# Optimization experiments

Measured on AMD Instinct MI355X. Metric: run time of the kernel, lower is better.

## Reference

```python
import jax, jax.numpy as jnp
import numpy as np

B, H, S, D = 2, 16, 2048, 64

def setup_inputs() -> dict:
    key = jax.random.key(0)
    kq, kk, kv = jax.random.split(key, 3)
    query = jax.random.normal(kq, (B, H, S, D), dtype=jnp.float32)
    key_t = jax.random.normal(kk, (B, H, S, D), dtype=jnp.float32)
    value = jax.random.normal(kv, (B, H, S, D), dtype=jnp.float32)
    return {"query": query, "key": key_t, "value": value}

def reference(query, key, value):
    d_k = query.shape[-1]
    scale = 1.0 / jnp.sqrt(jnp.asarray(d_k, dtype=query.dtype))
    # scores: [B, H, S, S]
    scores = jnp.einsum('bhqd,bhkd->bhqk', query, key) * scale
    p_attn = jax.nn.softmax(scores, axis=-1)
    output = jnp.einsum('bhqk,bhkd->bhqd', p_attn, value)
    return (output, p_attn)
```

## Files before the change

### kernel.cpp

```cpp
#include <hip/hip_runtime.h>

#define SS 2048
#define DD 64
#define QB 128
#define KVB 64
#define NT (SS / KVB)

typedef unsigned short ushort_t;
typedef __attribute__((ext_vector_type(4)))  float f32x4;
typedef __attribute__((ext_vector_type(16))) float f32x16;
typedef __attribute__((ext_vector_type(8)))  short bf16x8;
typedef __attribute__((ext_vector_type(2)))  unsigned int u32x2;

static __device__ __forceinline__ unsigned short f2bf(float f) {
    unsigned u = __builtin_bit_cast(unsigned, f);
    u += 0x7FFFu + ((u >> 16) & 1u);
    return (unsigned short)(u >> 16);
}

static __device__ __forceinline__ f32x16 zero16() {
    f32x16 z;
#pragma unroll
    for (int i = 0; i < 16; ++i) z[i] = 0.f;
    return z;
}

union PFrag { bf16x8 v; unsigned w[4]; };

#define GLL16(src, dst) \
    __builtin_amdgcn_global_load_lds((const __attribute__((address_space(1))) void*)(src), \
                                     (__attribute__((address_space(3))) void*)(dst), 16, 0, 0)

__global__ void cvt_bf16(const float* __restrict__ src, ushort_t* __restrict__ dst,
                         int n8, float scale)
{
    int i = blockIdx.x * blockDim.x + threadIdx.x;
    if (i >= n8) return;
    f32x4 a = ((const f32x4*)src)[2 * i];
    f32x4 b = ((const f32x4*)src)[2 * i + 1];
    bf16x8 o;
#pragma unroll
    for (int j = 0; j < 4; ++j) o[j] = (short)f2bf(a[j] * scale);
#pragma unroll
    for (int j = 0; j < 4; ++j) o[4 + j] = (short)f2bf(b[j] * scale);
    ((bf16x8*)dst)[i] = o;
}

__global__ void transposeV(const float* __restrict__ V, ushort_t* __restrict__ Vt)
{
    __shared__ float tile[64][65];
    const int tid = threadIdx.x;
    const int hh = blockIdx.x >> 5;
    const int kt = blockIdx.x & 31;

#pragma unroll
    for (int it = 0; it < 4; ++it) {
        int m = it * 256 + tid;
        int r = m >> 4, c4 = m & 15;
        f32x4 v = *(const f32x4*)(V + ((size_t)(hh * SS + kt * 64 + r)) * DD + c4 * 4);
#pragma unroll
        for (int j = 0; j < 4; ++j) tile[r][c4 * 4 + j] = v[j];
    }
    __syncthreads();
#pragma unroll
    for (int it = 0; it < 2; ++it) {
        int m = it * 256 + tid;
        int d = m >> 3, c8 = m & 7;
        bf16x8 o;
#pragma unroll
        for (int j = 0; j < 8; ++j) o[j] = (short)f2bf(tile[c8 * 8 + j][d]);
        *(bf16x8*)(Vt + ((size_t)hh * DD + d) * SS + kt * 64 + c8 * 8) = o;
    }
}

__global__ __launch_bounds__(256, 2)
void attn_main(const ushort_t* __restrict__ Qbf, const ushort_t* __restrict__ Kbf,
               const ushort_t* __restrict__ Vtbf, float* __restrict__ gO,
               float* __restrict__ gP)
{
    __shared__ ushort_t lds[2][8192];

    const int tid  = threadIdx.x;
    const int lane = tid & 63;
    const int wave = tid >> 6;
    const int lo5  = lane & 31;
    const int hi   = lane >> 5;

    const int bid  = blockIdx.x;
    const int wg   = (bid & 7) * 64 + (bid >> 3);
    const int head = wg >> 4;
    const int q0b  = (wg & 15) * QB;

    const ushort_t* Qh = Qbf  + (size_t)head * SS * DD;
    const ushort_t* Kh = Kbf  + (size_t)head * SS * DD;
    const ushort_t* Vh = Vtbf + (size_t)head * DD * SS;
    float* Oh = gO + (size_t)head * SS * DD;
    float* Ph = gP + (size_t)head * SS * SS;

    const int qg = q0b + wave * 32 + lo5;
    bf16x8 qf[4];
#pragma unroll
    for (int ks = 0; ks < 4; ++ks)
        qf[ks] = *(const bf16x8*)(Qh + (size_t)qg * DD + ks * 16 + hi * 8);

    const int lgrp = lane >> 3;
    const int lchk = (lane & 7) ^ lgrp;
    const ushort_t* srcK[2], *srcV[2];
    ushort_t* dK[2][2], *dV[2][2];
#pragma unroll
    for (int j = 0; j < 2; ++j) {
        int W = wave * 2 + j;
        srcK[j] = Kh + (size_t)(W * 8 + lgrp) * DD + lchk * 8;
        srcV[j] = Vh + (size_t)(W * 8 + lgrp) * SS + lchk * 8;
#pragma unroll
        for (int b = 0; b < 2; ++b) {
            dK[b][j] = &lds[b][W * 512];
            dV[b][j] = &lds[b][4096 + W * 512];
        }
    }

#pragma unroll
    for (int j = 0; j < 2; ++j) GLL16(srcK[j], dK[0][j]);
    __syncthreads();

    float lsum0 = 0.f, lsum1 = 0.f;
    int buf = 0;
    for (int t = 0; t < NT; ++t) {
        if (t + 1 < NT) {
#pragma unroll
            for (int j = 0; j < 2; ++j)
                GLL16(srcK[j] + (size_t)(t + 1) * KVB * DD, dK[buf ^ 1][j]);
        }
        const ushort_t* Ksb = &lds[buf][0];
#pragma unroll
        for (int sub = 0; sub < 2; ++sub) {
            f32x16 acc = zero16();
            int kvl = sub * 32 + lo5;
#pragma unroll
            for (int ks = 0; ks < 4; ++ks) {
                bf16x8 kf = *(const bf16x8*)(Ksb + kvl * 64 + ((((ks * 2) + hi) ^ (kvl & 7)) << 3));
                acc = __builtin_amdgcn_mfma_f32_32x32x16_bf16(kf, qf[ks], acc, 0, 0, 0);
            }
#pragma unroll
            for (int r = 0; r < 16; r += 2) {
                lsum0 += __builtin_exp2f(acc[r]);
                lsum1 += __builtin_exp2f(acc[r + 1]);
            }
        }
        __syncthreads();
        buf ^= 1;
    }
    float l_run = lsum0 + lsum1;
    l_run += __shfl_xor(l_run, 32);
    const float rinv = 1.0f / l_run;

    f32x16 o0 = zero16(), o1 = zero16();
    float* prow_base = Ph + (size_t)qg * SS;

#pragma unroll
    for (int j = 0; j < 2; ++j) { GLL16(srcK[j], dK[0][j]); GLL16(srcV[j], dV[0][j]); }
    __syncthreads();

    buf = 0;
    for (int t = 0; t < NT; ++t) {
        if (t + 1 < NT) {
#pragma unroll
            for (int j = 0; j < 2; ++j) {
                GLL16(srcK[j] + (size_t)(t + 1) * KVB * DD, dK[buf ^ 1][j]);
                GLL16(srcV[j] + (size_t)(t + 1) * KVB,      dV[buf ^ 1][j]);
            }
        }
        const ushort_t* Ksb = &lds[buf][0];
        const ushort_t* Vtb = &lds[buf][4096];
#pragma unroll
        for (int sub = 0; sub < 2; ++sub) {
            f32x16 acc = zero16();
            int kvl = sub * 32 + lo5;
#pragma unroll
            for (int ks = 0; ks < 4; ++ks) {
                bf16x8 kf = *(const bf16x8*)(Ksb + kvl * 64 + ((((ks * 2) + hi) ^ (kvl & 7)) << 3));
                acc = __builtin_amdgcn_mfma_f32_32x32x16_bf16(kf, qf[ks], acc, 0, 0, 0);
            }
            float pr[16];
#pragma unroll
            for (int r = 0; r < 16; ++r) pr[r] = __builtin_exp2f(acc[r]);

            float* prow = prow_base + t * KVB + sub * 32;
#pragma unroll
            for (int g = 0; g < 4; ++g) {
                f32x4 st = { pr[4*g+0] * rinv, pr[4*g+1] * rinv, pr[4*g+2] * rinv, pr[4*g+3] * rinv };
                *(f32x4*)(prow + g * 8 + hi * 4) = st;
            }

            unsigned u[8];
#pragma unroll
            for (int j = 0; j < 8; ++j)
                u[j] = (unsigned)f2bf(pr[2*j]) | ((unsigned)f2bf(pr[2*j+1]) << 16);

            unsigned s0 = __shfl_xor(u[0], 32), s1 = __shfl_xor(u[1], 32);
            unsigned s2 = __shfl_xor(u[2], 32), s3 = __shfl_xor(u[3], 32);
            unsigned s4 = __shfl_xor(u[4], 32), s5 = __shfl_xor(u[5], 32);
            unsigned s6 = __shfl_xor(u[6], 32), s7 = __shfl_xor(u[7], 32);
            PFrag pf0, pf1;
            pf0.w[0] = hi ? s2 : u[0];  pf0.w[1] = hi ? s3 : u[1];
            pf0.w[2] = hi ? u[2] : s0;  pf0.w[3] = hi ? u[3] : s1;
            pf1.w[0] = hi ? s6 : u[4];  pf1.w[1] = hi ? s7 : u[5];
            pf1.w[2] = hi ? u[6] : s4;  pf1.w[3] = hi ? u[7] : s5;

#pragma unroll
            for (int dt = 0; dt < 2; ++dt) {
                int drow = dt * 32 + lo5;
                int c0 = ((sub * 4) + 0 + hi) ^ (drow & 7);
                int c1 = ((sub * 4) + 2 + hi) ^ (drow & 7);
                bf16x8 vf0 = *(const bf16x8*)(Vtb + drow * 64 + (c0 << 3));
                bf16x8 vf1 = *(const bf16x8*)(Vtb + drow * 64 + (c1 << 3));
                f32x16& od = dt ? o1 : o0;
                od = __builtin_amdgcn_mfma_f32_32x32x16_bf16(vf0, pf0.v, od, 0, 0, 0);
                od = __builtin_amdgcn_mfma_f32_32x32x16_bf16(vf1, pf1.v, od, 0, 0, 0);
            }
        }
        __syncthreads();
        buf ^= 1;
    }

    float* orow = Oh + (size_t)qg * DD;
#pragma unroll
    for (int dt = 0; dt < 2; ++dt) {
        const f32x16& od = dt ? o1 : o0;
#pragma unroll
        for (int g = 0; g < 4; ++g) {
            f32x4 st = { od[4*g+0] * rinv, od[4*g+1] * rinv, od[4*g+2] * rinv, od[4*g+3] * rinv };
            *(f32x4*)(orow + dt * 32 + g * 8 + hi * 4) = st;
        }
    }
}

__global__ __launch_bounds__(256, 2)
void attn_fused(const float* __restrict__ gQ, const float* __restrict__ gK,
                const float* __restrict__ gV, float* __restrict__ gO,
                float* __restrict__ gP)
{
    __shared__ unsigned short Qs[QB * DD];
    __shared__ unsigned short Ks[KVB * DD];
    __shared__ unsigned short Vt[DD * KVB];

    const int tid  = threadIdx.x;
    const int lane = tid & 63;
    const int wave = tid >> 6;
    const int lo5  = lane & 31;
    const int hi   = lane >> 5;

    const int head = blockIdx.x >> 4;
    const int qblk = blockIdx.x & 15;
    const int q0b  = qblk * QB;

    const float* Qh = gQ + (size_t)head * SS * DD;
    const float* Kh = gK + (size_t)head * SS * DD;
    const float* Vh = gV + (size_t)head * SS * DD;
    float* Oh = gO + (size_t)head * SS * DD;
    float* Ph = gP + (size_t)head * SS * SS;

    const float SCALE = 0.125f * 1.44269504088896340736f;

#pragma unroll
    for (int it = 0; it < 8; ++it) {
        int m = it * 256 + tid;
        int q = m >> 4, d4 = m & 15;
        f32x4 v = *(const f32x4*)(Qh + (size_t)(q0b + q) * DD + d4 * 4);
        unsigned a = (unsigned)f2bf(v.x * SCALE) | ((unsigned)f2bf(v.y * SCALE) << 16);
        unsigned b = (unsigned)f2bf(v.z * SCALE) | ((unsigned)f2bf(v.w * SCALE) << 16);
        u32x2 w; w.x = a; w.y = b;
        *(u32x2*)(Qs + q * 64 + d4 * 4) = w;
    }
    __syncthreads();

    const int qrow = wave * 32 + lo5;
    bf16x8 qf[4];
#pragma unroll
    for (int ks = 0; ks < 4; ++ks)
        qf[ks] = *(const bf16x8*)(Qs + qrow * 64 + ks * 16 + hi * 8);

    auto stageK = [&](int kv0) {
#pragma unroll
        for (int it = 0; it < 4; ++it) {
            int m = it * 256 + tid;
            int kv = m >> 4, d4 = m & 15;
            f32x4 v = *(const f32x4*)(Kh + (size_t)(kv0 + kv) * DD + d4 * 4);
            unsigned a = (unsigned)f2bf(v.x) | ((unsigned)f2bf(v.y) << 16);
            unsigned b = (unsigned)f2bf(v.z) | ((unsigned)f2bf(v.w) << 16);
            int c16 = (d4 >> 1) ^ (kv & 7);
            u32x2 w; w.x = a; w.y = b;
            *(u32x2*)(Ks + kv * 64 + c16 * 8 + (d4 & 1) * 4) = w;
        }
    };
    auto stageV = [&](int kv0) {
#pragma unroll
        for (int it = 0; it < 2; ++it) {
            int m = it * 256 + tid;
            int kv2 = m >> 4, d4 = m & 15;
            const float* p0 = Vh + (size_t)(kv0 + kv2 * 2) * DD + d4 * 4;
            f32x4 v0 = *(const f32x4*)(p0);
            f32x4 v1 = *(const f32x4*)(p0 + DD);
#pragma unroll
            for (int c = 0; c < 4; ++c) {
                int d = d4 * 4 + c;
                unsigned u = (unsigned)f2bf(v0[c]) | ((unsigned)f2bf(v1[c]) << 16);
                int c16 = (kv2 >> 2) ^ (d & 7);
                *(unsigned*)(Vt + d * 64 + c16 * 8 + (kv2 & 3) * 2) = u;
            }
        }
    };

    float m_run = -1e30f, l_run = 0.f;
    for (int kv0 = 0; kv0 < SS; kv0 += KVB) {
        __syncthreads();
        stageK(kv0);
        __syncthreads();
#pragma unroll
        for (int sub = 0; sub < 2; ++sub) {
            f32x16 acc = zero16();
            int kvl = sub * 32 + lo5;
#pragma unroll
            for (int ks = 0; ks < 4; ++ks) {
                bf16x8 kf = *(const bf16x8*)(Ks + kvl * 64 + ((((ks * 2) + hi) ^ (kvl & 7)) << 3));
                acc = __builtin_amdgcn_mfma_f32_32x32x16_bf16(kf, qf[ks], acc, 0, 0, 0);
            }
            float tm = acc[0];
#pragma unroll
            for (int r = 1; r < 16; ++r) tm = fmaxf(tm, acc[r]);
            float mn = fmaxf(m_run, tm);
            float sum = 0.f;
#pragma unroll
            for (int r = 0; r < 16; ++r) sum += __builtin_exp2f(acc[r] - mn);
            l_run = l_run * __builtin_exp2f(m_run - mn) + sum;
            m_run = mn;
        }
    }
    {
        float mo = __shfl_xor(m_run, 32);
        float mf = fmaxf(m_run, mo);
        float la = l_run * __builtin_exp2f(m_run - mf);
        float lb = __shfl_xor(la, 32);
        l_run = la + lb;
        m_run = mf;
    }
    const float rinv = 1.0f / l_run;

    f32x16 o0 = zero16(), o1 = zero16();
    const int qg = q0b + wave * 32 + lo5;
    float* prow_base = Ph + (size_t)qg * SS;

    for (int kv0 = 0; kv0 < SS; kv0 += KVB) {
        __syncthreads();
        stageK(kv0);
        stageV(kv0);
        __syncthreads();
#pragma unroll
        for (int sub = 0; sub < 2; ++sub) {
            f32x16 acc = zero16();
            int kvl = sub * 32 + lo5;
#pragma unroll
            for (int ks = 0; ks < 4; ++ks) {
                bf16x8 kf = *(const bf16x8*)(Ks + kvl * 64 + ((((ks * 2) + hi) ^ (kvl & 7)) << 3));
                acc = __builtin_amdgcn_mfma_f32_32x32x16_bf16(kf, qf[ks], acc, 0, 0, 0);
            }
            float pr[16];
#pragma unroll
            for (int r = 0; r < 16; ++r) pr[r] = __builtin_exp2f(acc[r] - m_run);

            float* prow = prow_base + kv0 + sub * 32;
#pragma unroll
            for (int g = 0; g < 4; ++g) {
                f32x4 st = { pr[4*g+0] * rinv, pr[4*g+1] * rinv, pr[4*g+2] * rinv, pr[4*g+3] * rinv };
                *(f32x4*)(prow + g * 8 + hi * 4) = st;
            }

            unsigned u[8];
#pragma unroll
            for (int j = 0; j < 8; ++j)
                u[j] = (unsigned)f2bf(pr[2*j]) | ((unsigned)f2bf(pr[2*j+1]) << 16);

            unsigned s0 = __shfl_xor(u[0], 32), s1 = __shfl_xor(u[1], 32);
            unsigned s2 = __shfl_xor(u[2], 32), s3 = __shfl_xor(u[3], 32);
            unsigned s4 = __shfl_xor(u[4], 32), s5 = __shfl_xor(u[5], 32);
            unsigned s6 = __shfl_xor(u[6], 32), s7 = __shfl_xor(u[7], 32);
            PFrag pf0, pf1;
            pf0.w[0] = hi ? s2 : u[0];  pf0.w[1] = hi ? s3 : u[1];
            pf0.w[2] = hi ? u[2] : s0;  pf0.w[3] = hi ? u[3] : s1;
            pf1.w[0] = hi ? s6 : u[4];  pf1.w[1] = hi ? s7 : u[5];
            pf1.w[2] = hi ? u[6] : s4;  pf1.w[3] = hi ? u[7] : s5;

#pragma unroll
            for (int dt = 0; dt < 2; ++dt) {
                int drow = dt * 32 + lo5;
                int c0 = ((sub * 4) + 0 + hi) ^ (drow & 7);
                int c1 = ((sub * 4) + 2 + hi) ^ (drow & 7);
                bf16x8 vf0 = *(const bf16x8*)(Vt + drow * 64 + (c0 << 3));
                bf16x8 vf1 = *(const bf16x8*)(Vt + drow * 64 + (c1 << 3));
                f32x16& od = dt ? o1 : o0;
                od = __builtin_amdgcn_mfma_f32_32x32x16_bf16(vf0, pf0.v, od, 0, 0, 0);
                od = __builtin_amdgcn_mfma_f32_32x32x16_bf16(vf1, pf1.v, od, 0, 0, 0);
            }
        }
    }

    float* orow = Oh + (size_t)qg * DD;
#pragma unroll
    for (int dt = 0; dt < 2; ++dt) {
        const f32x16& od = dt ? o1 : o0;
#pragma unroll
        for (int g = 0; g < 4; ++g) {
            f32x4 st = { od[4*g+0] * rinv, od[4*g+1] * rinv, od[4*g+2] * rinv, od[4*g+3] * rinv };
            *(f32x4*)(orow + dt * 32 + g * 8 + hi * 4) = st;
        }
    }
}

extern "C" void kernel_launch(void* const* d_in, const int* in_sizes, int n_in,
                              void* d_out, int out_size, void* d_ws, size_t ws_size,
                              hipStream_t stream) {
    const float* Q = (const float*)d_in[0];
    const float* K = (const float*)d_in[1];
    const float* V = (const float*)d_in[2];
    float* O = (float*)d_out;
    float* P = O + (size_t)2 * 16 * SS * DD;

    const size_t HD = (size_t)32 * SS * DD;
    const size_t need = 3 * HD * sizeof(ushort_t);
    const float SCALE = 0.125f * 1.44269504088896340736f;

    if (ws_size >= need) {
        ushort_t* wsp  = (ushort_t*)d_ws;
        ushort_t* Qbf  = wsp;
        ushort_t* Kbf  = wsp + HD;
        ushort_t* Vtbf = wsp + 2 * HD;
        int n8 = (int)(HD / 8);
        hipLaunchKernelGGL(cvt_bf16, dim3(n8 / 256), dim3(256), 0, stream, Q, Qbf, n8, SCALE);
        hipLaunchKernelGGL(cvt_bf16, dim3(n8 / 256), dim3(256), 0, stream, K, Kbf, n8, 1.0f);
        hipLaunchKernelGGL(transposeV, dim3(1024), dim3(256), 0, stream, V, Vtbf);
        hipLaunchKernelGGL(attn_main, dim3(512), dim3(256), 0, stream, Qbf, Kbf, Vtbf, O, P);
    } else {
        hipLaunchKernelGGL(attn_fused, dim3(512), dim3(256), 0, stream, Q, K, V, O, P);
    }
}
```

Measured before the change: 215.2 us.

## Split KV range across waves with LDS reduction and fuse Q conversion

The main attention kernel now gives each block 32 query rows, and its four waves each take a quarter of the KV sequence. Softmax denominators and partial outputs are combined through LDS at the end. K and V fragments are read directly from global memory instead of through a double-buffered global_load_lds pipeline. Q bf16 conversion and scaling move inside the kernel, which drops a separate conversion launch, and P stores become nontemporal. The launch uses 2048 blocks with a 3-blocks-per-CU bound to raise parallelism, at the cost of uncached-by-LDS direct global K/V reads and an extra cross-wave reduction.

```diff
diff --git a/kernel.cpp b/kernel.cpp
--- a/kernel.cpp
+++ b/kernel.cpp
@@ -2,9 +2,6 @@
 
 #define SS 2048
 #define DD 64
-#define QB 128
-#define KVB 64
-#define NT (SS / KVB)
 
 typedef unsigned short ushort_t;
 typedef __attribute__((ext_vector_type(4)))  float f32x4;
@@ -26,10 +23,6 @@
 }
 
 union PFrag { bf16x8 v; unsigned w[4]; };
-
-#define GLL16(src, dst) \
-    __builtin_amdgcn_global_load_lds((const __attribute__((address_space(1))) void*)(src), \
-                                     (__attribute__((address_space(3))) void*)(dst), 16, 0, 0)
 
 __global__ void cvt_bf16(const float* __restrict__ src, ushort_t* __restrict__ dst,
                          int n8, float scale)
@@ -73,12 +66,13 @@
     }
 }
 
-__global__ __launch_bounds__(256, 2)
-void attn_main(const ushort_t* __restrict__ Qbf, const ushort_t* __restrict__ Kbf,
-               const ushort_t* __restrict__ Vtbf, float* __restrict__ gO,
-               float* __restrict__ gP)
+__global__ __launch_bounds__(256, 3)
+void attn_main2(const float* __restrict__ gQ, const ushort_t* __restrict__ Kbf,
+                const ushort_t* __restrict__ Vtbf, float* __restrict__ gO,
+                float* __restrict__ gP)
 {
-    __shared__ ushort_t lds[2][8192];
+    __shared__ float lsm[4 * 32];
+    __shared__ float osm[4 * 64 * 33];
 
     const int tid  = threadIdx.x;
     const int lane = tid & 63;
@@ -87,109 +81,85 @@
     const int hi   = lane >> 5;
 
     const int bid  = blockIdx.x;
-    const int wg   = (bid & 7) * 64 + (bid >> 3);
-    const int head = wg >> 4;
-    const int q0b  = (wg & 15) * QB;
-
-    const ushort_t* Qh = Qbf  + (size_t)head * SS * DD;
+    const int wg   = (bid & 7) * 256 + (bid >> 3);
+    const int head = wg >> 6;
+    const int q0b  = (wg & 63) * 32;
+
+    const float*    Qh = gQ   + (size_t)head * SS * DD;
     const ushort_t* Kh = Kbf  + (size_t)head * SS * DD;
     const ushort_t* Vh = Vtbf + (size_t)head * DD * SS;
     float* Oh = gO + (size_t)head * SS * DD;
     float* Ph = gP + (size_t)head * SS * SS;
 
-    const int qg = q0b + wave * 32 + lo5;
+    const float SCALE = 0.125f * 1.44269504088896340736f;
+
+    const int qrow = q0b + lo5;
     bf16x8 qf[4];
 #pragma unroll
-    for (int ks = 0; ks < 4; ++ks)
-        qf[ks] = *(const bf16x8*)(Qh + (size_t)qg * DD + ks * 16 + hi * 8);
-
-    const int lgrp = lane >> 3;
-    const int lchk = (lane & 7) ^ lgrp;
-    const ushort_t* srcK[2], *srcV[2];
-    ushort_t* dK[2][2], *dV[2][2];
-#pragma unroll
-    for (int j = 0; j < 2; ++j) {
-        int W = wave * 2 + j;
-        srcK[j] = Kh + (size_t)(W * 8 + lgrp) * DD + lchk * 8;
-        srcV[j] = Vh + (size_t)(W * 8 + lgrp) * SS + lchk * 8;
-#pragma unroll
-        for (int b = 0; b < 2; ++b) {
-            dK[b][j] = &lds[b][W * 512];
-            dV[b][j] = &lds[b][4096 + W * 512];
-        }
-    }
-
-#pragma unroll
-    for (int j = 0; j < 2; ++j) GLL16(srcK[j], dK[0][j]);
-    __syncthreads();
-
-    float lsum0 = 0.f, lsum1 = 0.f;
-    int buf = 0;
-    for (int t = 0; t < NT; ++t) {
-        if (t + 1 < NT) {
-#pragma unroll
-            for (int j = 0; j < 2; ++j)
-                GLL16(srcK[j] + (size_t)(t + 1) * KVB * DD, dK[buf ^ 1][j]);
-        }
-        const ushort_t* Ksb = &lds[buf][0];
+    for (int ks = 0; ks < 4; ++ks) {
+        const float* qp = Qh + (size_t)qrow * DD + ks * 16 + hi * 8;
+        f32x4 a = *(const f32x4*)(qp);
+        f32x4 b = *(const f32x4*)(qp + 4);
+        bf16x8 o;
+#pragma unroll
+        for (int j = 0; j < 4; ++j) o[j] = (short)f2bf(a[j] * SCALE);
+#pragma unroll
+        for (int j = 0; j < 4; ++j) o[4 + j] = (short)f2bf(b[j] * SCALE);
+        qf[ks] = o;
+    }
+
+    const int kv_base = wave * 512;
+
+    float ls0 = 0.f, ls1 = 0.f;
+#pragma unroll 2
+    for (int t = 0; t < 8; ++t) {
+        int kv0 = kv_base + t * 64;
 #pragma unroll
         for (int sub = 0; sub < 2; ++sub) {
             f32x16 acc = zero16();
-            int kvl = sub * 32 + lo5;
+            const ushort_t* kp = Kh + (size_t)(kv0 + sub * 32 + lo5) * DD + hi * 8;
 #pragma unroll
             for (int ks = 0; ks < 4; ++ks) {
-                bf16x8 kf = *(const bf16x8*)(Ksb + kvl * 64 + ((((ks * 2) + hi) ^ (kvl & 7)) << 3));
+                bf16x8 kf = *(const bf16x8*)(kp + ks * 16);
                 acc = __builtin_amdgcn_mfma_f32_32x32x16_bf16(kf, qf[ks], acc, 0, 0, 0);
             }
 #pragma unroll
             for (int r = 0; r < 16; r += 2) {
-                lsum0 += __builtin_exp2f(acc[r]);
-                lsum1 += __builtin_exp2f(acc[r + 1]);
-            }
-        }
-        __syncthreads();
-        buf ^= 1;
-    }
-    float l_run = lsum0 + lsum1;
-    l_run += __shfl_xor(l_run, 32);
-    const float rinv = 1.0f / l_run;
+                ls0 += __builtin_exp2f(acc[r]);
+                ls1 += __builtin_exp2f(acc[r + 1]);
+            }
+        }
+    }
+    float lsum = ls0 + ls1;
+    lsum += __shfl_xor(lsum, 32);
+    lsm[wave * 32 + lo5] = lsum;
+    __syncthreads();
+    const float rinv = 1.0f / (lsm[lo5] + lsm[32 + lo5] + lsm[64 + lo5] + lsm[96 + lo5]);
 
     f32x16 o0 = zero16(), o1 = zero16();
-    float* prow_base = Ph + (size_t)qg * SS;
-
-#pragma unroll
-    for (int j = 0; j < 2; ++j) { GLL16(srcK[j], dK[0][j]); GLL16(srcV[j], dV[0][j]); }
-    __syncthreads();
-
-    buf = 0;
-    for (int t = 0; t < NT; ++t) {
-        if (t + 1 < NT) {
-#pragma unroll
-            for (int j = 0; j < 2; ++j) {
-                GLL16(srcK[j] + (size_t)(t + 1) * KVB * DD, dK[buf ^ 1][j]);
-                GLL16(srcV[j] + (size_t)(t + 1) * KVB,      dV[buf ^ 1][j]);
-            }
-        }
-        const ushort_t* Ksb = &lds[buf][0];
-        const ushort_t* Vtb = &lds[buf][4096];
+    float* prow_base = Ph + (size_t)qrow * SS;
+
+#pragma unroll 2
+    for (int t = 0; t < 8; ++t) {
+        int kv0 = kv_base + t * 64;
 #pragma unroll
         for (int sub = 0; sub < 2; ++sub) {
             f32x16 acc = zero16();
-            int kvl = sub * 32 + lo5;
+            const ushort_t* kp = Kh + (size_t)(kv0 + sub * 32 + lo5) * DD + hi * 8;
 #pragma unroll
             for (int ks = 0; ks < 4; ++ks) {
-                bf16x8 kf = *(const bf16x8*)(Ksb + kvl * 64 + ((((ks * 2) + hi) ^ (kvl & 7)) << 3));
+                bf16x8 kf = *(const bf16x8*)(kp + ks * 16);
                 acc = __builtin_amdgcn_mfma_f32_32x32x16_bf16(kf, qf[ks], acc, 0, 0, 0);
             }
             float pr[16];
 #pragma unroll
             for (int r = 0; r < 16; ++r) pr[r] = __builtin_exp2f(acc[r]);
 
-            float* prow = prow_base + t * KVB + sub * 32;
+            float* prow = prow_base + kv0 + sub * 32;
 #pragma unroll
             for (int g = 0; g < 4; ++g) {
                 f32x4 st = { pr[4*g+0] * rinv, pr[4*g+1] * rinv, pr[4*g+2] * rinv, pr[4*g+3] * rinv };
-                *(f32x4*)(prow + g * 8 + hi * 4) = st;
+                __builtin_nontemporal_store(st, (f32x4*)(prow + g * 8 + hi * 4));
             }
 
             unsigned u[8];
@@ -209,29 +179,46 @@
 
 #pragma unroll
             for (int dt = 0; dt < 2; ++dt) {
-                int drow = dt * 32 + lo5;
-                int c0 = ((sub * 4) + 0 + hi) ^ (drow & 7);
-                int c1 = ((sub * 4) + 2 + hi) ^ (drow & 7);
-                bf16x8 vf0 = *(const bf16x8*)(Vtb + drow * 64 + (c0 << 3));
-                bf16x8 vf1 = *(const bf16x8*)(Vtb + drow * 64 + (c1 << 3));
+                const ushort_t* vp = Vh + (size_t)(dt * 32 + lo5) * SS + kv0 + sub * 32 + hi * 8;
+                bf16x8 vf0 = *(const bf16x8*)(vp);
+                bf16x8 vf1 = *(const bf16x8*)(vp + 16);
                 f32x16& od = dt ? o1 : o0;
                 od = __builtin_amdgcn_mfma_f32_32x32x16_bf16(vf0, pf0.v, od, 0, 0, 0);
                 od = __builtin_amdgcn_mfma_f32_32x32x16_bf16(vf1, pf1.v, od, 0, 0, 0);
             }
         }
-        __syncthreads();
-        buf ^= 1;
-    }
-
-    float* orow = Oh + (size_t)qg * DD;
+    }
+
 #pragma unroll
     for (int dt = 0; dt < 2; ++dt) {
         const f32x16& od = dt ? o1 : o0;
 #pragma unroll
         for (int g = 0; g < 4; ++g) {
-            f32x4 st = { od[4*g+0] * rinv, od[4*g+1] * rinv, od[4*g+2] * rinv, od[4*g+3] * rinv };
-            *(f32x4*)(orow + dt * 32 + g * 8 + hi * 4) = st;
-        }
+#pragma unroll
+            for (int j = 0; j < 4; ++j) {
+                int d = dt * 32 + g * 8 + hi * 4 + j;
+                osm[(wave * 64 + d) * 33 + lo5] = od[4 * g + j];
+            }
+        }
+    }
+    __syncthreads();
+
+    {
+        const int q  = tid >> 3;
+        const int d0 = (tid & 7) * 8;
+        const float rq = 1.0f / (lsm[q] + lsm[32 + q] + lsm[64 + q] + lsm[96 + q]);
+        float out[8];
+#pragma unroll
+        for (int i = 0; i < 8; ++i) {
+            int d = d0 + i;
+            out[i] = (osm[(0 * 64 + d) * 33 + q] + osm[(1 * 64 + d) * 33 + q] +
+                      osm[(2 * 64 + d) * 33 + q] + osm[(3 * 64 + d) * 33 + q]) * rq;
+        }
+        float* op = Oh + (size_t)(q0b + q) * DD + d0;
+        f32x4 a = { out[0], out[1], out[2], out[3] };
+        f32x4 b = { out[4], out[5], out[6], out[7] };
+        *(f32x4*)(op)     = a;
+        *(f32x4*)(op + 4) = b;
     }
 }
 
@@ -240,9 +227,9 @@
                 const float* __restrict__ gV, float* __restrict__ gO,
                 float* __restrict__ gP)
 {
-    __shared__ unsigned short Qs[QB * DD];
-    __shared__ unsigned short Ks[KVB * DD];
-    __shared__ unsigned short Vt[DD * KVB];
+    __shared__ unsigned short Qs[128 * DD];
+    __shared__ unsigned short Ks[64 * DD];
+    __shared__ unsigned short Vt[DD * 64];
 
     const int tid  = threadIdx.x;
     const int lane = tid & 63;
@@ -251,8 +238,7 @@
     const int hi   = lane >> 5;
 
     const int head = blockIdx.x >> 4;
-    const int qblk = blockIdx.x & 15;
-    const int q0b  = qblk * QB;
+    const int q0b  = (blockIdx.x & 15) * 128;
 
     const float* Qh = gQ + (size_t)head * SS * DD;
     const float* Kh = gK + (size_t)head * SS * DD;
@@ -312,7 +298,7 @@
     };
 
     float m_run = -1e30f, l_run = 0.f;
-    for (int kv0 = 0; kv0 < SS; kv0 += KVB) {
+    for (int kv0 = 0; kv0 < SS; kv0 += 64) {
         __syncthreads();
         stageK(kv0);
         __syncthreads();
@@ -350,7 +336,7 @@
     const int qg = q0b + wave * 32 + lo5;
     float* prow_base = Ph + (size_t)qg * SS;
 
-    for (int kv0 = 0; kv0 < SS; kv0 += KVB) {
+    for (int kv0 = 0; kv0 < SS; kv0 += 64) {
         __syncthreads();
         stageK(kv0);
         stageV(kv0);
@@ -426,19 +412,15 @@
     float* P = O + (size_t)2 * 16 * SS * DD;
 
     const size_t HD = (size_t)32 * SS * DD;
-    const size_t need = 3 * HD * sizeof(ushort_t);
-    const float SCALE = 0.125f * 1.44269504088896340736f;
+    const size_t need = 2 * HD * sizeof(ushort_t);
 
     if (ws_size >= need) {
-        ushort_t* wsp  = (ushort_t*)d_ws;
-        ushort_t* Qbf  = wsp;
-        ushort_t* Kbf  = wsp + HD;
-        ushort_t* Vtbf = wsp + 2 * HD;
+        ushort_t* Kbf  = (ushort_t*)d_ws;
+        ushort_t* Vtbf = Kbf + HD;
         int n8 = (int)(HD / 8);
-        hipLaunchKernelGGL(cvt_bf16, dim3(n8 / 256), dim3(256), 0, stream, Q, Qbf, n8, SCALE);
         hipLaunchKernelGGL(cvt_bf16, dim3(n8 / 256), dim3(256), 0, stream, K, Kbf, n8, 1.0f);
         hipLaunchKernelGGL(transposeV, dim3(1024), dim3(256), 0, stream, V, Vtbf);
-        hipLaunchKernelGGL(attn_main, dim3(512), dim3(256), 0, stream, Qbf, Kbf, Vtbf, O, P);
+        hipLaunchKernelGGL(attn_main2, dim3(2048), dim3(256), 0, stream, Q, Kbf, Vtbf, O, P);
     } else {
         hipLaunchKernelGGL(attn_fused, dim3(512), dim3(256), 0, stream, Q, K, V, O, P);
     }
```

Result: slower. 517.3 us (+140.4%).
